# Performance work log

Hardware: AMD Instinct MI355X
Metric: run time of the kernel (lower is better)

## Reference

```python
import jax, jax.numpy as jnp
import numpy as np

N, E, IN_C, HEADS, OUT_C = 50000, 800000, 256, 8, 32
NEG_SLOPE = 0.2
BN_EPS = 1e-5


def setup_inputs() -> dict:
    key = jax.random.key(0)
    ks = jax.random.split(key, 12)
    x = jax.random.normal(ks[0], (N, IN_C), jnp.float32)
    edge_index = jax.random.randint(ks[1], (2, E), 0, N, dtype=jnp.int32)
    edge_attr = jax.random.uniform(ks[2], (E, 1), jnp.float32)
    s = 0.1
    W = jax.random.normal(ks[3], (IN_C, HEADS * OUT_C), jnp.float32) * s
    att_src = jax.random.normal(ks[4], (HEADS, OUT_C), jnp.float32) * s
    att_dst = jax.random.normal(ks[5], (HEADS, OUT_C), jnp.float32) * s
    W_edge = jax.random.normal(ks[6], (1, HEADS * OUT_C), jnp.float32) * s
    att_edge = jax.random.normal(ks[7], (HEADS, OUT_C), jnp.float32) * s
    bias = jnp.zeros((HEADS * OUT_C,), jnp.float32)
    gamma = jnp.ones((HEADS * OUT_C,), jnp.float32)
    beta = jnp.zeros((HEADS * OUT_C,), jnp.float32)
    return {"x": x, "edge_index": edge_index, "edge_attr": edge_attr, "W": W,
            "att_src": att_src, "att_dst": att_dst, "W_edge": W_edge,
            "att_edge": att_edge, "bias": bias, "gamma": gamma, "beta": beta}


def reference(x, edge_index, edge_attr, W, att_src, att_dst, W_edge, att_edge, bias, gamma, beta):
    # --- add self loops (fill_value='mean' for edge_attr, PyG GATConv default) ---
    loops = jnp.arange(N, dtype=edge_index.dtype)
    src = jnp.concatenate([edge_index[0], loops])      # [E+N]
    dst = jnp.concatenate([edge_index[1], loops])      # [E+N]
    ea_mean = jnp.mean(edge_attr, axis=0, keepdims=True)
    ea = jnp.concatenate([edge_attr, jnp.broadcast_to(ea_mean, (N, edge_attr.shape[1]))], axis=0)

    # --- linear projections ---
    h = (x @ W).reshape(N, HEADS, OUT_C)               # [N,H,C]
    a_src = jnp.einsum('nhc,hc->nh', h, att_src)       # [N,H]
    a_dst = jnp.einsum('nhc,hc->nh', h, att_dst)       # [N,H]
    he = (ea @ W_edge).reshape(-1, HEADS, OUT_C)       # [E+N,H,C]
    a_edge = jnp.einsum('ehc,hc->eh', he, att_edge)    # [E+N,H]

    # --- edge-wise attention logits + segment softmax over destination nodes ---
    alpha = jax.nn.leaky_relu(a_src[src] + a_dst[dst] + a_edge, NEG_SLOPE)  # [E+N,H]
    amax = jax.ops.segment_max(alpha, dst, num_segments=N)  # every node has a self loop
    alpha = jnp.exp(alpha - amax[dst])
    asum = jax.ops.segment_sum(alpha, dst, num_segments=N)
    alpha = alpha / (asum[dst] + 1e-16)

    # --- weighted aggregation (attention dropout is identity in eval) ---
    msg = alpha[:, :, None] * h[src]                   # [E+N,H,C]
    out = jax.ops.segment_sum(msg, dst, num_segments=N).reshape(N, HEADS * OUT_C) + bias

    # --- BatchNorm (batch stats) + ELU; feature dropout is identity in eval ---
    mean = jnp.mean(out, axis=0)
    var = jnp.var(out, axis=0)
    out = (out - mean) * jax.lax.rsqrt(var + BN_EPS) * gamma + beta
    return jax.nn.elu(out)
```

## Files before the change

kernel.cpp:

```cpp
#include <hip/hip_runtime.h>
#include <hip/hip_bf16.h>
#include <math.h>

#define HEADS 8
#define OUTC 32
#define INC 256
#define OC 256
#define NEG_SLOPE 0.2f
#define BN_EPS 1e-5f
#define HS_STRIDE 264

typedef __attribute__((ext_vector_type(8))) short short8;
typedef __attribute__((ext_vector_type(4))) float floatx4;

__device__ __forceinline__ float bf2f(ushort u) {
    union { uint i; float f; } c; c.i = ((uint)u) << 16; return c.f;
}
__device__ __forceinline__ ushort f2bf(float f) {
    union { float f; uint i; } c; c.f = f;
    uint i = c.i + 0x7fffu + ((c.i >> 16) & 1u);
    return (ushort)(i >> 16);
}
__device__ __forceinline__ float loadf(const void* src, int t, uint flag) {
    return flag ? bf2f(((const ushort*)src)[t]) : ((const float*)src)[t];
}
__device__ __forceinline__ uint dtype_flag(const uint* gamma_raw) {
    return gamma_raw[0] != 0x3F800000u ? 1u : 0u;
}

__global__ void k_transpose_w(const void* __restrict__ W, ushort* __restrict__ WT,
                              const uint* __restrict__ graw) {
    uint flag = dtype_flag(graw);
    int k = blockIdx.x;
    int n = threadIdx.x;
    float v = loadf(W, k * OC + n, flag);
    WT[(size_t)n * INC + k] = f2bf(v);
}

__global__ void k_prep(const void* __restrict__ att_src, const void* __restrict__ att_dst,
                       const void* __restrict__ gamma, const void* __restrict__ beta,
                       const void* __restrict__ We, const void* __restrict__ ae,
                       float* __restrict__ attS, float* __restrict__ attD,
                       float* __restrict__ gam, float* __restrict__ bet,
                       float* __restrict__ cvals) {
    uint flag = dtype_flag((const uint*)gamma);
    int t = threadIdx.x;
    attS[t] = loadf(att_src, t, flag);
    attD[t] = loadf(att_dst, t, flag);
    gam[t]  = loadf(gamma, t, flag);
    bet[t]  = loadf(beta, t, flag);
    __shared__ float s[OC];
    s[t] = loadf(We, t, flag) * loadf(ae, t, flag);
    __syncthreads();
    if (t < HEADS) {
        float v = 0.f;
        #pragma unroll
        for (int j = 0; j < OUTC; j++) v += s[t * OUTC + j];
        cvals[t] = v;
    }
}

__global__ void k_ea_reduce(const void* __restrict__ ea, int E, float* __restrict__ easum,
                            const uint* __restrict__ graw) {
    uint flag = dtype_flag(graw);
    int t = blockIdx.x * blockDim.x + threadIdx.x;
    float v = 0.f;
    for (int i = t; i < E; i += gridDim.x * blockDim.x) v += loadf(ea, i, flag);
    #pragma unroll
    for (int off = 32; off; off >>= 1) v += __shfl_down(v, off, 64);
    if ((threadIdx.x & 63) == 0) atomicAdd(easum, v);
}

__global__ void __launch_bounds__(256, 2) k_gemm(const void* __restrict__ xraw,
                                                 const ushort* __restrict__ WT,
                                                 ushort* __restrict__ Hb,
                                                 const float* __restrict__ attS,
                                                 const float* __restrict__ attD,
                                                 float* __restrict__ asrc,
                                                 float* __restrict__ adst,
                                                 int N, const uint* __restrict__ graw) {
    uint flag = dtype_flag(graw);
    __shared__ ushort hs[16 * HS_STRIDE];
    int wave = threadIdx.x >> 6;
    int lane = threadIdx.x & 63;
    int m = lane & 15, q = lane >> 4;

    short8 bfr[4][8];
    #pragma unroll
    for (int i = 0; i < 4; i++) {
        const short8* wb = (const short8*)(WT + (size_t)((wave * 4 + i) * 16 + m) * INC);
        #pragma unroll
        for (int kk = 0; kk < 8; kk++) bfr[i][kk] = wb[kk * 4 + q];
    }

    int tiles = (N + 15) >> 4;
    for (int rt = blockIdx.x; rt < tiles; rt += gridDim.x) {
        int row0 = rt << 4;
        __syncthreads();
        #pragma unroll
        for (int c = 0; c < 2; c++) {
            int ch = threadIdx.x * 2 + c;
            int r = ch >> 5, seg = ch & 31;
            int row = row0 + r; if (row > N - 1) row = N - 1;
            short8 v;
            if (flag) {
                v = *(const short8*)((const ushort*)xraw + (size_t)row * INC + seg * 8);
            } else {
                const float4* xf = (const float4*)((const float*)xraw + (size_t)row * INC + seg * 8);
                float4 f0 = xf[0], f1 = xf[1];
                v[0] = (short)f2bf(f0.x); v[1] = (short)f2bf(f0.y);
                v[2] = (short)f2bf(f0.z); v[3] = (short)f2bf(f0.w);
                v[4] = (short)f2bf(f1.x); v[5] = (short)f2bf(f1.y);
                v[6] = (short)f2bf(f1.z); v[7] = (short)f2bf(f1.w);
            }
            *(short8*)(hs + r * HS_STRIDE + seg * 8) = v;
        }
        __syncthreads();
        short8 afr[8];
        #pragma unroll
        for (int kk = 0; kk < 8; kk++)
            afr[kk] = *(const short8*)(hs + m * HS_STRIDE + kk * 32 + q * 8);
        __syncthreads();
        floatx4 acc[4];
        #pragma unroll
        for (int i = 0; i < 4; i++) {
            floatx4 a = {0.f, 0.f, 0.f, 0.f};
            #pragma unroll
            for (int kk = 0; kk < 8; kk++)
                a = __builtin_amdgcn_mfma_f32_16x16x32_bf16(afr[kk], bfr[i][kk], a, 0, 0, 0);
            acc[i] = a;
        }
        #pragma unroll
        for (int i = 0; i < 4; i++) {
            int col = (wave * 4 + i) * 16 + m;
            #pragma unroll
            for (int r4 = 0; r4 < 4; r4++)
                hs[(q * 4 + r4) * HS_STRIDE + col] = f2bf(acc[i][r4]);
        }
        __syncthreads();
        #pragma unroll
        for (int c = 0; c < 2; c++) {
            int ch = threadIdx.x * 2 + c;
            int r = ch >> 5, seg = ch & 31;
            int row = row0 + r;
            if (row < N) {
                short8 v = *(const short8*)(hs + r * HS_STRIDE + seg * 8);
                *(short8*)(Hb + (size_t)row * OC + seg * 8) = v;
            }
        }
        if (threadIdx.x < 128) {
            int lr = threadIdx.x >> 3, hd = threadIdx.x & 7;
            int n = row0 + lr;
            if (n < N) {
                const ushort4* hrow = (const ushort4*)(hs + lr * HS_STRIDE + hd * OUTC);
                const float* as = attS + hd * OUTC;
                const float* ad = attD + hd * OUTC;
                float s1 = 0.f, s2 = 0.f;
                #pragma unroll
                for (int c4 = 0; c4 < 8; c4++) {
                    ushort4 u = hrow[c4];
                    float v0 = bf2f(u.x), v1 = bf2f(u.y), v2 = bf2f(u.z), v3 = bf2f(u.w);
                    s1 += v0 * as[c4*4+0] + v1 * as[c4*4+1] + v2 * as[c4*4+2] + v3 * as[c4*4+3];
                    s2 += v0 * ad[c4*4+0] + v1 * ad[c4*4+1] + v2 * ad[c4*4+2] + v3 * ad[c4*4+3];
                }
                asrc[n * HEADS + hd] = s1;
                adst[n * HEADS + hd] = s2;
            }
        }
    }
}

__global__ void k_deginit(int* __restrict__ deg, int N) {
    int t = blockIdx.x * 256 + threadIdx.x;
    if (t < N) deg[t] = 1;
}
__global__ void k_hist(const int* __restrict__ ei, int E, int* __restrict__ deg) {
    int t = blockIdx.x * 256 + threadIdx.x;
    if (t < E) atomicAdd(&deg[ei[E + t]], 1);
}

__global__ void k_scan_local(const int* __restrict__ deg, int* __restrict__ part,
                             int* __restrict__ bsum, int N) {
    __shared__ int sth[256];
    int b = blockIdx.x, t = threadIdx.x;
    int base = b * 1024 + t * 4;
    int v0 = 0, v1 = 0, v2 = 0, v3 = 0;
    if (base + 0 < N) v0 = deg[base + 0];
    if (base + 1 < N) v1 = deg[base + 1];
    if (base + 2 < N) v2 = deg[base + 2];
    if (base + 3 < N) v3 = deg[base + 3];
    int tsum = v0 + v1 + v2 + v3;
    sth[t] = tsum;
    __syncthreads();
    #pragma unroll
    for (int off = 1; off < 256; off <<= 1) {
        int x = (t >= off) ? sth[t - off] : 0;
        __syncthreads();
        sth[t] += x;
        __syncthreads();
    }
    int excl = sth[t] - tsum;
    if (base + 0 < N) part[base + 0] = excl;
    if (base + 1 < N) part[base + 1] = excl + v0;
    if (base + 2 < N) part[base + 2] = excl + v0 + v1;
    if (base + 3 < N) part[base + 3] = excl + v0 + v1 + v2;
    if (t == 255) bsum[b] = sth[255];
}

__global__ void k_scan_blocks(const int* __restrict__ bsum, int* __restrict__ boff,
                              int nb, int* __restrict__ total) {
    __shared__ int sdata[256];
    __shared__ int carry;
    int t = threadIdx.x;
    if (t == 0) carry = 0;
    __syncthreads();
    for (int base = 0; base < nb; base += 256) {
        int v = (base + t < nb) ? bsum[base + t] : 0;
        sdata[t] = v;
        __syncthreads();
        #pragma unroll
        for (int off = 1; off < 256; off <<= 1) {
            int x = (t >= off) ? sdata[t - off] : 0;
            __syncthreads();
            sdata[t] += x;
            __syncthreads();
        }
        if (base + t < nb) boff[base + t] = carry + sdata[t] - v;
        __syncthreads();
        if (t == 255) carry += sdata[255];
        __syncthreads();
    }
    if (t == 0) total[0] = carry;
}

__global__ void k_scan_add(const int* __restrict__ part, const int* __restrict__ boff,
                           const int* __restrict__ total, int* __restrict__ rowstart,
                           int* __restrict__ cursor, int N) {
    int t = blockIdx.x * 256 + threadIdx.x;
    if (t < N) {
        int v = part[t] + boff[t >> 10];
        rowstart[t] = v;
        cursor[t]   = v;
    }
    if (t == 0) rowstart[N] = total[0];
}

__global__ void k_scatter(const int* __restrict__ ei, const void* __restrict__ eattr,
                          const float* __restrict__ easum, int* __restrict__ cursor,
                          uint* __restrict__ cpk, int E, int N,
                          const uint* __restrict__ graw) {
    uint flag = dtype_flag(graw);
    int t = blockIdx.x * 256 + threadIdx.x;
    if (t >= E + N) return;
    int s, d; float ea;
    if (t < E) { s = ei[t]; d = ei[E + t]; ea = loadf(eattr, t, flag); }
    else       { s = t - E; d = s;         ea = easum[0] / (float)E; }
    int pos = atomicAdd(&cursor[d], 1);
    cpk[pos] = ((uint)f2bf(ea) << 16) | ((uint)s & 0xFFFFu);
}

__global__ void __launch_bounds__(256) k_aggf(const int* __restrict__ rowstart,
                                              const uint* __restrict__ cpk,
                                              const float* __restrict__ asrc,
                                              const float* __restrict__ adst,
                                              const float* __restrict__ cvals,
                                              const ushort* __restrict__ Hb,
                                              ushort* __restrict__ outpre, int N) {
    int d = blockIdx.x * 4 + (threadIdx.x >> 6);
    if (d >= N) return;
    int lane = threadIdx.x & 63;
    int hd = lane >> 3;
    float ad = adst[d * HEADS + hd];
    float ch = cvals[hd];
    int beg = __builtin_amdgcn_readfirstlane(rowstart[d]);
    int end = __builtin_amdgcn_readfirstlane(rowstart[d + 1]);
    int l8 = lane & 7;
    float4 acc = {0.f, 0.f, 0.f, 0.f};
    float psum = 0.f;
    int j = beg;
    for (; j + 8 <= end; j += 8) {
        uint epack = cpk[j + l8];
        int sk[8]; float eaf[8];
        #pragma unroll
        for (int k = 0; k < 8; k++) {
            uint e = (uint)__builtin_amdgcn_readlane((int)epack, k);
            sk[k] = (int)(e & 0xFFFFu);
            eaf[k] = bf2f((ushort)(e >> 16));
        }
        ushort4 u[8]; float a[8];
        #pragma unroll
        for (int k = 0; k < 8; k++)
            u[k] = *(const ushort4*)(Hb + (size_t)sk[k] * OC + lane * 4);
        #pragma unroll
        for (int k = 0; k < 8; k++)
            a[k] = asrc[sk[k] * HEADS + hd];
        #pragma unroll
        for (int k = 0; k < 8; k++) {
            float l = (a[k] + ad) + eaf[k] * ch;
            l = fmaxf(l, NEG_SLOPE * l);
            float pe = __expf(l);
            psum += pe;
            acc.x += pe * bf2f(u[k].x); acc.y += pe * bf2f(u[k].y);
            acc.z += pe * bf2f(u[k].z); acc.w += pe * bf2f(u[k].w);
        }
    }
    int rem = end - j;
    if (rem > 0) {
        int jj = j + l8; if (jj > end - 1) jj = end - 1;
        uint epack = cpk[jj];
        int sk[8]; float eaf[8];
        #pragma unroll
        for (int k = 0; k < 8; k++) {
            uint e = (uint)__builtin_amdgcn_readlane((int)epack, k);
            sk[k] = (int)(e & 0xFFFFu);
            eaf[k] = bf2f((ushort)(e >> 16));
        }
        ushort4 u[8]; float a[8];
        #pragma unroll
        for (int k = 0; k < 8; k++)
            u[k] = *(const ushort4*)(Hb + (size_t)sk[k] * OC + lane * 4);
        #pragma unroll
        for (int k = 0; k < 8; k++)
            a[k] = asrc[sk[k] * HEADS + hd];
        #pragma unroll
        for (int k = 0; k < 8; k++) {
            float l = (a[k] + ad) + eaf[k] * ch;
            l = fmaxf(l, NEG_SLOPE * l);
            float pe = (k < rem) ? __expf(l) : 0.f;
            psum += pe;
            acc.x += pe * bf2f(u[k].x); acc.y += pe * bf2f(u[k].y);
            acc.z += pe * bf2f(u[k].z); acc.w += pe * bf2f(u[k].w);
        }
    }
    float inv = 1.f / (psum + 1e-16f);
    ushort4 o;
    o.x = f2bf(acc.x * inv); o.y = f2bf(acc.y * inv);
    o.z = f2bf(acc.z * inv); o.w = f2bf(acc.w * inv);
    *(ushort4*)(outpre + (size_t)d * OC + lane * 4) = o;
}

__global__ void __launch_bounds__(256) k_bnstats(const ushort* __restrict__ outpre,
                                                 float* __restrict__ stats, int N) {
    int t = threadIdx.x;
    int lane = t & 63, rr = t >> 6;
    int f4 = lane * 4;
    float r1[4] = {0.f, 0.f, 0.f, 0.f};
    float r2[4] = {0.f, 0.f, 0.f, 0.f};
    for (int n0 = blockIdx.x * 16 + rr * 4; n0 < N; n0 += gridDim.x * 16) {
        ushort4 u[4];
        #pragma unroll
        for (int j = 0; j < 4; j++) {
            int n = n0 + j;
            ushort4 z = {0, 0, 0, 0};
            u[j] = (n < N) ? *(const ushort4*)(outpre + (size_t)n * OC + f4) : z;
        }
        #pragma unroll
        for (int j = 0; j < 4; j++) {
            float v0 = bf2f(u[j].x), v1 = bf2f(u[j].y), v2 = bf2f(u[j].z), v3 = bf2f(u[j].w);
            r1[0] += v0; r2[0] += v0 * v0;
            r1[1] += v1; r2[1] += v1 * v1;
            r1[2] += v2; r2[2] += v2 * v2;
            r1[3] += v3; r2[3] += v3 * v3;
        }
    }
    __shared__ float sred[8][256];
    float4 a1 = {r1[0], r1[1], r1[2], r1[3]};
    float4 a2 = {r2[0], r2[1], r2[2], r2[3]};
    *(float4*)&sred[rr][f4]     = a1;
    *(float4*)&sred[4 + rr][f4] = a2;
    __syncthreads();
    float s1 = sred[0][t] + sred[1][t] + sred[2][t] + sred[3][t];
    float s2 = sred[4][t] + sred[5][t] + sred[6][t] + sred[7][t];
    atomicAdd(&stats[t], s1);
    atomicAdd(&stats[OC + t], s2);
}

__global__ void k_bnelu(const ushort* __restrict__ outpre, const float* __restrict__ stats,
                        const float* __restrict__ gamma, const float* __restrict__ beta,
                        void* __restrict__ out, int N, const uint* __restrict__ graw) {
    uint flag = dtype_flag(graw);
    int t = blockIdx.x * 256 + threadIdx.x;
    if (t >= N * (OC / 4)) return;
    int n = t >> 6, f4 = (t & 63) * 4;
    float invN = 1.f / (float)N;
    ushort4 u = *(const ushort4*)(outpre + (size_t)n * OC + f4);
    float r[4] = {bf2f(u.x), bf2f(u.y), bf2f(u.z), bf2f(u.w)};
    #pragma unroll
    for (int j = 0; j < 4; j++) {
        int f = f4 + j;
        float mean = stats[f] * invN;
        float var  = stats[OC + f] * invN - mean * mean;
        float xv = (r[j] - mean) * rsqrtf(var + BN_EPS) * gamma[f] + beta[f];
        r[j] = xv > 0.f ? xv : expm1f(xv);
    }
    if (flag) {
        ushort4 o; o.x = f2bf(r[0]); o.y = f2bf(r[1]); o.z = f2bf(r[2]); o.w = f2bf(r[3]);
        *(ushort4*)((ushort*)out + (size_t)n * OC + f4) = o;
    } else {
        float4 o; o.x = r[0]; o.y = r[1]; o.z = r[2]; o.w = r[3];
        *(float4*)((float*)out + (size_t)n * OC + f4) = o;
    }
}

extern "C" void kernel_launch(void* const* d_in, const int* in_sizes, int n_in,
                              void* d_out, int out_size, void* d_ws, size_t ws_size,
                              hipStream_t stream) {
    const void* x        = d_in[0];
    const int*  ei       = (const int*)d_in[1];
    const void* eattr    = d_in[2];
    const void* W        = d_in[3];
    const void* att_src  = d_in[4];
    const void* att_dst  = d_in[5];
    const void* W_edge   = d_in[6];
    const void* att_edge = d_in[7];
    const void* gamma    = d_in[9];
    const void* beta     = d_in[10];
    const uint* graw     = (const uint*)gamma;

    int N = in_sizes[0] / INC;
    int E = in_sizes[1] / 2;
    int T = E + N;
    int nb = (N + 1023) / 1024;

    char* ws = (char*)d_ws;
    size_t off = 0;
    auto alloc = [&](size_t bytes) -> void* {
        void* pp = ws + off;
        off += (bytes + 255) & ~(size_t)255;
        return pp;
    };
    ushort* WT       = (ushort*)alloc((size_t)INC * OC * 2);
    float*  attS     = (float*)alloc(OC * 4);
    float*  attD     = (float*)alloc(OC * 4);
    float*  gam      = (float*)alloc(OC * 4);
    float*  bet      = (float*)alloc(OC * 4);
    ushort* Hb       = (ushort*)alloc((size_t)N * OC * 2);
    float*  asrc     = (float*)alloc((size_t)N * HEADS * 4);
    float*  adst     = (float*)alloc((size_t)N * HEADS * 4);
    int*    deg      = (int*)alloc((size_t)N * 4);
    int*    part     = (int*)alloc((size_t)N * 4);
    int*    bsum     = (int*)alloc((size_t)(nb + 1) * 4);
    int*    boff     = (int*)alloc((size_t)(nb + 1) * 4);
    int*    total    = (int*)alloc(256);
    int*    rowstart = (int*)alloc((size_t)(N + 1) * 4);
    int*    cursor   = (int*)alloc((size_t)N * 4);
    uint*   cpk      = (uint*)alloc((size_t)T * 4);
    ushort* outpre   = (ushort*)alloc((size_t)N * OC * 2);
    float*  stats    = (float*)alloc(2 * OC * 4);
    float*  easum    = (float*)alloc(256);
    float*  cvals    = (float*)alloc(256);

    hipMemsetAsync(stats, 0, 2 * OC * 4, stream);
    hipMemsetAsync(easum, 0, 4, stream);

    k_transpose_w<<<INC, OC, 0, stream>>>(W, WT, graw);
    k_prep<<<1, 256, 0, stream>>>(att_src, att_dst, gamma, beta, W_edge, att_edge,
                                  attS, attD, gam, bet, cvals);
    k_ea_reduce<<<512, 256, 0, stream>>>(eattr, E, easum, graw);

    k_deginit<<<(N + 255) / 256, 256, 0, stream>>>(deg, N);
    k_hist<<<(E + 255) / 256, 256, 0, stream>>>(ei, E, deg);
    k_scan_local<<<nb, 256, 0, stream>>>(deg, part, bsum, N);
    k_scan_blocks<<<1, 256, 0, stream>>>(bsum, boff, nb, total);
    k_scan_add<<<(N + 255) / 256, 256, 0, stream>>>(part, boff, total, rowstart, cursor, N);
    k_scatter<<<(T + 255) / 256, 256, 0, stream>>>(ei, eattr, easum, cursor, cpk, E, N, graw);

    int tiles = (N + 15) / 16;
    int gblocks = tiles < 512 ? tiles : 512;
    k_gemm<<<gblocks, 256, 0, stream>>>(x, WT, Hb, attS, attD, asrc, adst, N, graw);
    k_aggf<<<(N + 3) / 4, 256, 0, stream>>>(rowstart, cpk, asrc, adst, cvals, Hb, outpre, N);
    k_bnstats<<<512, 256, 0, stream>>>(outpre, stats, N);
    k_bnelu<<<(N * (OC / 4) + 255) / 256, 256, 0, stream>>>(outpre, stats, gam, bet,
                                                            d_out, N, graw);
}
```

Measured before the change: 398.4 us.

## Merge setup kernels, launch one GEMM tile per block, precompute BN scale/shift

Fuses the weight transpose, parameter prep, edge-attr reduction and degree histogram into a single multi-role setup kernel. The self-loop degree is now added in the scan, with a memset replacing the init kernel. The GEMM launches one 16-row tile per block and reloads the W fragments in every block, where before a persistent grid reused them. BN+ELU precomputes per-feature scale and shift in shared memory and uses a grid-stride loop. The aim is fewer launches and less per-element work, at the cost of more redundant weight loads in the GEMM.

```diff
diff --git a/kernel.cpp b/kernel.cpp
--- a/kernel.cpp
+++ b/kernel.cpp
@@ -28,47 +28,47 @@
     return gamma_raw[0] != 0x3F800000u ? 1u : 0u;
 }
 
-__global__ void k_transpose_w(const void* __restrict__ W, ushort* __restrict__ WT,
-                              const uint* __restrict__ graw) {
-    uint flag = dtype_flag(graw);
-    int k = blockIdx.x;
-    int n = threadIdx.x;
-    float v = loadf(W, k * OC + n, flag);
-    WT[(size_t)n * INC + k] = f2bf(v);
-}
-
-__global__ void k_prep(const void* __restrict__ att_src, const void* __restrict__ att_dst,
-                       const void* __restrict__ gamma, const void* __restrict__ beta,
-                       const void* __restrict__ We, const void* __restrict__ ae,
-                       float* __restrict__ attS, float* __restrict__ attD,
-                       float* __restrict__ gam, float* __restrict__ bet,
-                       float* __restrict__ cvals) {
+__global__ void k_setup(const void* __restrict__ W, ushort* __restrict__ WT,
+                        const void* __restrict__ att_src, const void* __restrict__ att_dst,
+                        const void* __restrict__ gamma, const void* __restrict__ beta,
+                        const void* __restrict__ We, const void* __restrict__ ae,
+                        float* __restrict__ attS, float* __restrict__ attD,
+                        float* __restrict__ gam, float* __restrict__ bet,
+                        float* __restrict__ cvals, float* __restrict__ stats,
+                        const void* __restrict__ eattr, const int* __restrict__ ei,
+                        float* __restrict__ easum, int* __restrict__ deg, int E) {
     uint flag = dtype_flag((const uint*)gamma);
-    int t = threadIdx.x;
-    attS[t] = loadf(att_src, t, flag);
-    attD[t] = loadf(att_dst, t, flag);
-    gam[t]  = loadf(gamma, t, flag);
-    bet[t]  = loadf(beta, t, flag);
-    __shared__ float s[OC];
-    s[t] = loadf(We, t, flag) * loadf(ae, t, flag);
-    __syncthreads();
-    if (t < HEADS) {
+    int b = blockIdx.x, t = threadIdx.x;
+    if (b < 256) {
+        float v = loadf(W, b * OC + t, flag);
+        WT[(size_t)t * INC + b] = f2bf(v);
+    } else if (b == 256) {
+        attS[t] = loadf(att_src, t, flag);
+        attD[t] = loadf(att_dst, t, flag);
+        gam[t]  = loadf(gamma, t, flag);
+        bet[t]  = loadf(beta, t, flag);
+        stats[t] = 0.f;
+        stats[OC + t] = 0.f;
+        __shared__ float s[OC];
+        s[t] = loadf(We, t, flag) * loadf(ae, t, flag);
+        __syncthreads();
+        if (t < HEADS) {
+            float v = 0.f;
+            #pragma unroll
+            for (int j = 0; j < OUTC; j++) v += s[t * OUTC + j];
+            cvals[t] = v;
+        }
+    } else {
+        int eb = b - 257;
         float v = 0.f;
-        #pragma unroll
-        for (int j = 0; j < OUTC; j++) v += s[t * OUTC + j];
-        cvals[t] = v;
-    }
-}
-
-__global__ void k_ea_reduce(const void* __restrict__ ea, int E, float* __restrict__ easum,
-                            const uint* __restrict__ graw) {
-    uint flag = dtype_flag(graw);
-    int t = blockIdx.x * blockDim.x + threadIdx.x;
-    float v = 0.f;
-    for (int i = t; i < E; i += gridDim.x * blockDim.x) v += loadf(ea, i, flag);
-    #pragma unroll
-    for (int off = 32; off; off >>= 1) v += __shfl_down(v, off, 64);
-    if ((threadIdx.x & 63) == 0) atomicAdd(easum, v);
+        for (int i = eb * 256 + t; i < E; i += 512 * 256) {
+            v += loadf(eattr, i, flag);
+            atomicAdd(&deg[ei[E + i]], 1);
+        }
+        #pragma unroll
+        for (int off = 32; off; off >>= 1) v += __shfl_down(v, off, 64);
+        if ((t & 63) == 0) atomicAdd(easum, v);
+    }
 }
 
 __global__ void __launch_bounds__(256, 2) k_gemm(const void* __restrict__ xraw,
@@ -93,90 +93,77 @@
         for (int kk = 0; kk < 8; kk++) bfr[i][kk] = wb[kk * 4 + q];
     }
 
-    int tiles = (N + 15) >> 4;
-    for (int rt = blockIdx.x; rt < tiles; rt += gridDim.x) {
-        int row0 = rt << 4;
-        __syncthreads();
-        #pragma unroll
-        for (int c = 0; c < 2; c++) {
-            int ch = threadIdx.x * 2 + c;
-            int r = ch >> 5, seg = ch & 31;
-            int row = row0 + r; if (row > N - 1) row = N - 1;
-            short8 v;
-            if (flag) {
-                v = *(const short8*)((const ushort*)xraw + (size_t)row * INC + seg * 8);
-            } else {
-                const float4* xf = (const float4*)((const float*)xraw + (size_t)row * INC + seg * 8);
-                float4 f0 = xf[0], f1 = xf[1];
-                v[0] = (short)f2bf(f0.x); v[1] = (short)f2bf(f0.y);
-                v[2] = (short)f2bf(f0.z); v[3] = (short)f2bf(f0.w);
-                v[4] = (short)f2bf(f1.x); v[5] = (short)f2bf(f1.y);
-                v[6] = (short)f2bf(f1.z); v[7] = (short)f2bf(f1.w);
+    int row0 = blockIdx.x << 4;
+    #pragma unroll
+    for (int c = 0; c < 2; c++) {
+        int ch = threadIdx.x * 2 + c;
+        int r = ch >> 5, seg = ch & 31;
+        int row = row0 + r; if (row > N - 1) row = N - 1;
+        short8 v;
+        if (flag) {
+            v = *(const short8*)((const ushort*)xraw + (size_t)row * INC + seg * 8);
+        } else {
+            const float4* xf = (const float4*)((const float*)xraw + (size_t)row * INC + seg * 8);
+            float4 f0 = xf[0], f1 = xf[1];
+            v[0] = (short)f2bf(f0.x); v[1] = (short)f2bf(f0.y);
+            v[2] = (short)f2bf(f0.z); v[3] = (short)f2bf(f0.w);
+            v[4] = (short)f2bf(f1.x); v[5] = (short)f2bf(f1.y);
+            v[6] = (short)f2bf(f1.z); v[7] = (short)f2bf(f1.w);
+        }
+        *(short8*)(hs + r * HS_STRIDE + seg * 8) = v;
+    }
+    __syncthreads();
+    short8 afr[8];
+    #pragma unroll
+    for (int kk = 0; kk < 8; kk++)
+        afr[kk] = *(const short8*)(hs + m * HS_STRIDE + kk * 32 + q * 8);
+    __syncthreads();
+    floatx4 acc[4];
+    #pragma unroll
+    for (int i = 0; i < 4; i++) {
+        floatx4 a = {0.f, 0.f, 0.f, 0.f};
+        #pragma unroll
+        for (int kk = 0; kk < 8; kk++)
+            a = __builtin_amdgcn_mfma_f32_16x16x32_bf16(afr[kk], bfr[i][kk], a, 0, 0, 0);
+        acc[i] = a;
+    }
+    #pragma unroll
+    for (int i = 0; i < 4; i++) {
+        int col = (wave * 4 + i) * 16 + m;
+        #pragma unroll
+        for (int r4 = 0; r4 < 4; r4++)
+            hs[(q * 4 + r4) * HS_STRIDE + col] = f2bf(acc[i][r4]);
+    }
+    __syncthreads();
+    #pragma unroll
+    for (int c = 0; c < 2; c++) {
+        int ch = threadIdx.x * 2 + c;
+        int r = ch >> 5, seg = ch & 31;
+        int row = row0 + r;
+        if (row < N) {
+            short8 v = *(const short8*)(hs + r * HS_STRIDE + seg * 8);
+            *(short8*)(Hb + (size_t)row * OC + seg * 8) = v;
+        }
+    }
+    if (threadIdx.x < 128) {
+        int lr = threadIdx.x >> 3, hd = threadIdx.x & 7;
+        int n = row0 + lr;
+        if (n < N) {
+            const ushort4* hrow = (const ushort4*)(hs + lr * HS_STRIDE + hd * OUTC);
+            const float* as = attS + hd * OUTC;
+            const float* ad = attD + hd * OUTC;
+            float s1 = 0.f, s2 = 0.f;
+            #pragma unroll
+            for (int c4 = 0; c4 < 8; c4++) {
+                ushort4 u = hrow[c4];
+                float v0 = bf2f(u.x), v1 = bf2f(u.y), v2 = bf2f(u.z), v3 = bf2f(u.w);
+                s1 += v0 * as[c4*4+0] + v1 * as[c4*4+1] + v2 * as[c4*4+2] + v3 * as[c4*4+3];
+                s2 += v0 * ad[c4*4+0] + v1 * ad[c4*4+1] + v2 * ad[c4*4+2] + v3 * ad[c4*4+3];
             }
-            *(short8*)(hs + r * HS_STRIDE + seg * 8) = v;
-        }
-        __syncthreads();
-        short8 afr[8];
-        #pragma unroll
-        for (int kk = 0; kk < 8; kk++)
-            afr[kk] = *(const short8*)(hs + m * HS_STRIDE + kk * 32 + q * 8);
-        __syncthreads();
-        floatx4 acc[4];
-        #pragma unroll
-        for (int i = 0; i < 4; i++) {
-            floatx4 a = {0.f, 0.f, 0.f, 0.f};
-            #pragma unroll
-            for (int kk = 0; kk < 8; kk++)
-                a = __builtin_amdgcn_mfma_f32_16x16x32_bf16(afr[kk], bfr[i][kk], a, 0, 0, 0);
-            acc[i] = a;
-        }
-        #pragma unroll
-        for (int i = 0; i < 4; i++) {
-            int col = (wave * 4 + i) * 16 + m;
-            #pragma unroll
-            for (int r4 = 0; r4 < 4; r4++)
-                hs[(q * 4 + r4) * HS_STRIDE + col] = f2bf(acc[i][r4]);
-        }
-        __syncthreads();
-        #pragma unroll
-        for (int c = 0; c < 2; c++) {
-            int ch = threadIdx.x * 2 + c;
-            int r = ch >> 5, seg = ch & 31;
-            int row = row0 + r;
-            if (row < N) {
-                short8 v = *(const short8*)(hs + r * HS_STRIDE + seg * 8);
-                *(short8*)(Hb + (size_t)row * OC + seg * 8) = v;
-            }
-        }
-        if (threadIdx.x < 128) {
-            int lr = threadIdx.x >> 3, hd = threadIdx.x & 7;
-            int n = row0 + lr;
-            if (n < N) {
-                const ushort4* hrow = (const ushort4*)(hs + lr * HS_STRIDE + hd * OUTC);
-                const float* as = attS + hd * OUTC;
-                const float* ad = attD + hd * OUTC;
-                float s1 = 0.f, s2 = 0.f;
-                #pragma unroll
-                for (int c4 = 0; c4 < 8; c4++) {
-                    ushort4 u = hrow[c4];
-                    float v0 = bf2f(u.x), v1 = bf2f(u.y), v2 = bf2f(u.z), v3 = bf2f(u.w);
-                    s1 += v0 * as[c4*4+0] + v1 * as[c4*4+1] + v2 * as[c4*4+2] + v3 * as[c4*4+3];
-                    s2 += v0 * ad[c4*4+0] + v1 * ad[c4*4+1] + v2 * ad[c4*4+2] + v3 * ad[c4*4+3];
-                }
-                asrc[n * HEADS + hd] = s1;
-                adst[n * HEADS + hd] = s2;
-            }
-        }
-    }
-}
-
-__global__ void k_deginit(int* __restrict__ deg, int N) {
-    int t = blockIdx.x * 256 + threadIdx.x;
-    if (t < N) deg[t] = 1;
-}
-__global__ void k_hist(const int* __restrict__ ei, int E, int* __restrict__ deg) {
-    int t = blockIdx.x * 256 + threadIdx.x;
-    if (t < E) atomicAdd(&deg[ei[E + t]], 1);
+            asrc[n * HEADS + hd] = s1;
+            adst[n * HEADS + hd] = s2;
+        }
+    }
 }
 
 __global__ void k_scan_local(const int* __restrict__ deg, int* __restrict__ part,
@@ -185,10 +172,10 @@
     int b = blockIdx.x, t = threadIdx.x;
     int base = b * 1024 + t * 4;
     int v0 = 0, v1 = 0, v2 = 0, v3 = 0;
-    if (base + 0 < N) v0 = deg[base + 0];
-    if (base + 1 < N) v1 = deg[base + 1];
-    if (base + 2 < N) v2 = deg[base + 2];
-    if (base + 3 < N) v3 = deg[base + 3];
+    if (base + 0 < N) v0 = deg[base + 0] + 1;
+    if (base + 1 < N) v1 = deg[base + 1] + 1;
+    if (base + 2 < N) v2 = deg[base + 2] + 1;
+    if (base + 3 < N) v3 = deg[base + 3] + 1;
     int tsum = v0 + v1 + v2 + v3;
     sth[t] = tsum;
     __syncthreads();
@@ -375,30 +362,45 @@
     atomicAdd(&stats[OC + t], s2);
 }
 
-__global__ void k_bnelu(const ushort* __restrict__ outpre, const float* __restrict__ stats,
-                        const float* __restrict__ gamma, const float* __restrict__ beta,
-                        void* __restrict__ out, int N, const uint* __restrict__ graw) {
+__global__ void __launch_bounds__(256) k_bnelu(const ushort* __restrict__ outpre,
+                                               const float* __restrict__ stats,
+                                               const float* __restrict__ gam,
+                                               const float* __restrict__ bet,
+                                               void* __restrict__ out, int N,
+                                               const uint* __restrict__ graw) {
     uint flag = dtype_flag(graw);
-    int t = blockIdx.x * 256 + threadIdx.x;
-    if (t >= N * (OC / 4)) return;
-    int n = t >> 6, f4 = (t & 63) * 4;
-    float invN = 1.f / (float)N;
-    ushort4 u = *(const ushort4*)(outpre + (size_t)n * OC + f4);
-    float r[4] = {bf2f(u.x), bf2f(u.y), bf2f(u.z), bf2f(u.w)};
-    #pragma unroll
-    for (int j = 0; j < 4; j++) {
-        int f = f4 + j;
-        float mean = stats[f] * invN;
-        float var  = stats[OC + f] * invN - mean * mean;
-        float xv = (r[j] - mean) * rsqrtf(var + BN_EPS) * gamma[f] + beta[f];
-        r[j] = xv > 0.f ? xv : expm1f(xv);
-    }
-    if (flag) {
-        ushort4 o; o.x = f2bf(r[0]); o.y = f2bf(r[1]); o.z = f2bf(r[2]); o.w = f2bf(r[3]);
-        *(ushort4*)((ushort*)out + (size_t)n * OC + f4) = o;
-    } else {
-        float4 o; o.x = r[0]; o.y = r[1]; o.z = r[2]; o.w = r[3];
-        *(float4*)((float*)out + (size_t)n * OC + f4) = o;
+    __shared__ float sc[OC], sh[OC];
+    int t = threadIdx.x;
+    {
+        float invN = 1.f / (float)N;
+        float mean = stats[t] * invN;
+        float var  = stats[OC + t] * invN - mean * mean;
+        float s = rsqrtf(var + BN_EPS) * gam[t];
+        sc[t] = s;
+        sh[t] = bet[t] - mean * s;
+    }
+    __syncthreads();
+    int lane = t & 63, rr = t >> 6;
+    int f4 = lane * 4;
+    float s0 = sc[f4 + 0], s1 = sc[f4 + 1], s2 = sc[f4 + 2], s3 = sc[f4 + 3];
+    float h0 = sh[f4 + 0], h1 = sh[f4 + 1], h2 = sh[f4 + 2], h3 = sh[f4 + 3];
+    for (int n = blockIdx.x * 4 + rr; n < N; n += gridDim.x * 4) {
+        ushort4 u = *(const ushort4*)(outpre + (size_t)n * OC + f4);
+        float r0 = bf2f(u.x) * s0 + h0;
+        float r1 = bf2f(u.y) * s1 + h1;
+        float r2 = bf2f(u.z) * s2 + h2;
+        float r3 = bf2f(u.w) * s3 + h3;
+        r0 = r0 > 0.f ? r0 : expm1f(r0);
+        r1 = r1 > 0.f ? r1 : expm1f(r1);
+        r2 = r2 > 0.f ? r2 : expm1f(r2);
+        r3 = r3 > 0.f ? r3 : expm1f(r3);
+        if (flag) {
+            ushort4 o; o.x = f2bf(r0); o.y = f2bf(r1); o.z = f2bf(r2); o.w = f2bf(r3);
+            *(ushort4*)((ushort*)out + (size_t)n * OC + f4) = o;
+        } else {
+            float4 o; o.x = r0; o.y = r1; o.z = r2; o.w = r3;
+            *(float4*)((float*)out + (size_t)n * OC + f4) = o;
+        }
     }
 }
 
@@ -450,26 +452,21 @@
     float*  easum    = (float*)alloc(256);
     float*  cvals    = (float*)alloc(256);
 
-    hipMemsetAsync(stats, 0, 2 * OC * 4, stream);
     hipMemsetAsync(easum, 0, 4, stream);
-
-    k_transpose_w<<<INC, OC, 0, stream>>>(W, WT, graw);
-    k_prep<<<1, 256, 0, stream>>>(att_src, att_dst, gamma, beta, W_edge, att_edge,
-                                  attS, attD, gam, bet, cvals);
-    k_ea_reduce<<<512, 256, 0, stream>>>(eattr, E, easum, graw);
-
-    k_deginit<<<(N + 255) / 256, 256, 0, stream>>>(deg, N);
-    k_hist<<<(E + 255) / 256, 256, 0, stream>>>(ei, E, deg);
+    hipMemsetAsync(deg, 0, (size_t)N * 4, stream);
+
+    k_setup<<<769, 256, 0, stream>>>(W, WT, att_src, att_dst, gamma, beta, W_edge,
+                                     att_edge, attS, attD, gam, bet, cvals, stats,
+                                     eattr, ei, easum, deg, E);
+
     k_scan_local<<<nb, 256, 0, stream>>>(deg, part, bsum, N);
     k_scan_blocks<<<1, 256, 0, stream>>>(bsum, boff, nb, total);
     k_scan_add<<<(N + 255) / 256, 256, 0, stream>>>(part, boff, total, rowstart, cursor, N);
     k_scatter<<<(T + 255) / 256, 256, 0, stream>>>(ei, eattr, easum, cursor, cpk, E, N, graw);
 
     int tiles = (N + 15) / 16;
-    int gblocks = tiles < 512 ? tiles : 512;
-    k_gemm<<<gblocks, 256, 0, stream>>>(x, WT, Hb, attS, attD, asrc, adst, N, graw);
+    k_gemm<<<tiles, 256, 0, stream>>>(x, WT, Hb, attS, attD, asrc, adst, N, graw);
     k_aggf<<<(N + 3) / 4, 256, 0, stream>>>(rowstart, cpk, asrc, adst, cvals, Hb, outpre, N);
     k_bnstats<<<512, 256, 0, stream>>>(outpre, stats, N);
-    k_bnelu<<<(N * (OC / 4) + 255) / 256, 256, 0, stream>>>(outpre, stats, gam, bet,
-                                                            d_out, N, graw);
-}
+    k_bnelu<<<512, 256, 0, stream>>>(outpre, stats, gam, bet, d_out, N, graw);
+}
```

Result: faster. 375.2 us (-5.8%).
